# Kernel optimization log

Measured on AMD Instinct MI355X. Metric: run time of the kernel, lower is better.

The kernel has to match this reference:

```python
import jax, jax.numpy as jnp
import numpy as np

SR = 44100.0
MIN_GAIN, MAX_GAIN = -48.0, 12.0
MIN_EQ, MAX_EQ = -15.0, 15.0
MIN_CTS, MAX_CTS = -20.0, 10.0
# Freeverb (JUCE Reverb, as used by pedalboard.Reverb) tunings @ 44.1 kHz
COMB_T = [1116, 1188, 1277, 1356, 1422, 1491, 1557, 1617]
AP_T = [556, 441, 341, 225]
COMB_OFF = [0]
for _L in COMB_T:
    COMB_OFF.append(COMB_OFF[-1] + _L)
AP_OFF = [0]
for _L in AP_T:
    AP_OFF.append(AP_OFF[-1] + _L)


def restore(x, lo, hi):
    # inverse of normalize-to-(0,1)
    return x * (hi - lo) + lo


def first_order(fc, kind):
    # bilinear-transform 1st-order HP/LP (pedalboard High/LowpassFilter are 1st order)
    K = jnp.tan(np.pi * fc / SR)
    a1 = (K - 1.0) / (K + 1.0)
    z = jnp.zeros_like(fc)
    if kind == "hp":
        b0 = 1.0 / (1.0 + K)
        b = jnp.stack([b0, -b0, z], -1)
    else:
        b0 = K / (1.0 + K)
        b = jnp.stack([b0, b0, z], -1)
    a = jnp.stack([jnp.ones_like(fc), a1, z], -1)
    return b, a


def shelf(fc, gain_db, high):
    # RBJ cookbook shelf, Q = 1/sqrt(2)
    A = 10.0 ** (gain_db / 40.0)
    w = 2.0 * np.pi * fc / SR
    cw = jnp.cos(w)
    alpha = jnp.sin(w) * (np.sqrt(2.0) / 2.0)
    sq = 2.0 * jnp.sqrt(A) * alpha
    s = 1.0 if high else -1.0
    b0 = A * ((A + 1.0) + s * (A - 1.0) * cw + sq)
    b1 = -2.0 * s * A * ((A - 1.0) + s * (A + 1.0) * cw)
    b2 = A * ((A + 1.0) + s * (A - 1.0) * cw - sq)
    a0 = (A + 1.0) - s * (A - 1.0) * cw + sq
    a1 = 2.0 * s * ((A - 1.0) - s * (A + 1.0) * cw)
    a2 = (A + 1.0) - s * (A - 1.0) * cw - sq
    return jnp.stack([b0, b1, b2], -1), jnp.stack([a0, a1, a2], -1)


def peak(fc, gain_db, q):
    # RBJ cookbook peaking EQ
    A = 10.0 ** (gain_db / 40.0)
    w = 2.0 * np.pi * fc / SR
    cw = jnp.cos(w)
    alpha = jnp.sin(w) / (2.0 * q)
    b = jnp.stack([1.0 + alpha * A, -2.0 * cw, 1.0 - alpha * A], -1)
    a = jnp.stack([1.0 + alpha / A, -2.0 * cw, 1.0 - alpha / A], -1)
    return b, a


def cascade_biquads(x, B, A):
    # x: [N, T]; B, A: [N, 6, 3]. DF2T cascade of 6 sections via one scan.
    B = B / A[..., :1]
    A = A / A[..., :1]
    n_sec = B.shape[1]

    def step(z, xt):  # z: [N, 6, 2], xt: [N]
        s = xt
        zn = []
        for k in range(n_sec):
            y = B[:, k, 0] * s + z[:, k, 0]
            z1 = B[:, k, 1] * s - A[:, k, 1] * y + z[:, k, 1]
            z2 = B[:, k, 2] * s - A[:, k, 2] * y
            zn.append(jnp.stack([z1, z2], -1))
            s = y
        return jnp.stack(zn, 1), s

    z0 = jnp.zeros((x.shape[0], n_sec, 2), x.dtype)
    _, y = jax.lax.scan(step, z0, x.T)
    return y.T


def compressor(x, thr_db, ratio, att_ms, rel_ms):
    # feed-forward compressor, dB-domain gain computer + one-pole attack/release
    a_att = jnp.exp(-1.0 / (att_ms * 1e-3 * SR))  # [N]
    a_rel = jnp.exp(-1.0 / (rel_ms * 1e-3 * SR))
    lvl = 20.0 * jnp.log10(jnp.abs(x) + 1e-6)  # [N, T]
    tgt = jnp.minimum(0.0, (thr_db[:, None] - lvl) * (1.0 - 1.0 / ratio[:, None]))

    def step(g, t):  # g, t: [N] gain reduction in dB (<= 0)
        coef = jnp.where(t < g, a_att, a_rel)
        g = coef * g + (1.0 - coef) * t
        return g, g

    _, g = jax.lax.scan(step, jnp.zeros(x.shape[0], x.dtype), tgt.T)
    return x * 10.0 ** (g.T / 20.0)


def freeverb(x, room, damp01, wet, dry, width):
    # JUCE/Freeverb mono: 8 parallel damped combs -> 4 series allpasses
    fb = room * 0.28 + 0.7
    damp = damp01 * 0.4
    wet1 = 3.0 * wet * 0.5 * (1.0 + width)
    dryg = 2.0 * dry
    N = x.shape[0]
    CL, AL = COMB_OFF[-1], AP_OFF[-1]

    def step(carry, xt):
        cb, ab, st, t = carry
        inp = xt * 0.015
        acc = jnp.zeros_like(xt)
        st_new = []
        for k in range(8):
            idx = COMB_OFF[k] + t % COMB_T[k]
            out = cb[:, idx]
            s = out * (1.0 - damp) + st[:, k] * damp
            cb = cb.at[:, idx].set(inp + s * fb)
            st_new.append(s)
            acc = acc + out
        for k in range(4):
            idx = AP_OFF[k] + t % AP_T[k]
            buf = ab[:, idx]
            ab = ab.at[:, idx].set(acc + buf * 0.5)
            acc = buf - acc
        y = acc * wet1 + xt * dryg
        return (cb, ab, jnp.stack(st_new, 1), t + 1), y

    carry0 = (jnp.zeros((N, CL), x.dtype), jnp.zeros((N, AL), x.dtype),
              jnp.zeros((N, 8), x.dtype), jnp.int32(0))
    _, y = jax.lax.scan(step, carry0, x.T)
    return y.T


def _forward(x, p):
    bs, nt, T = x.shape
    N = bs * nt
    xf = x.reshape(N, T)
    pf = p.reshape(N, 24)

    gain_in = restore(pf[:, 0], MIN_GAIN, MAX_GAIN)
    xf = xf * (10.0 ** (gain_in / 20.0))[:, None]

    hp_fc = restore(pf[:, 1], 0.0, 350.0)
    lp_fc = restore(pf[:, 2], 3000.0, 22000.0)
    hs_fc = restore(pf[:, 3], 1500.0, 16000.0)
    hs_g = restore(pf[:, 4], MIN_EQ, MAX_EQ)
    ls_fc = restore(pf[:, 5], 30.0, 450.0)
    ls_g = restore(pf[:, 6], MIN_EQ, MAX_EQ)
    mh_fc = restore(pf[:, 7], 600.0, 7000.0)
    mh_g = restore(pf[:, 8], MIN_EQ, MAX_EQ)
    mh_q = restore(pf[:, 9], 0.5, 3.0)
    ml_fc = restore(pf[:, 10], 200.0, 2500.0)
    ml_g = restore(pf[:, 11], MIN_EQ, MAX_EQ)
    ml_q = restore(pf[:, 12], 0.5, 3.0)
    c_thr = restore(pf[:, 13], MIN_CTS, MAX_CTS)
    c_rat = restore(pf[:, 14], 1.0, 20.0)
    c_att = restore(pf[:, 15], 1.0, 30.0)
    c_rel = restore(pf[:, 16], 100.0, 4000.0)

    coefs = [first_order(hp_fc, "hp"), first_order(lp_fc, "lp"),
             shelf(hs_fc, hs_g, True), shelf(ls_fc, ls_g, False),
             peak(mh_fc, mh_g, mh_q), peak(ml_fc, ml_g, ml_q)]
    B = jnp.stack([c[0] for c in coefs], 1)  # [N, 6, 3]
    A = jnp.stack([c[1] for c in coefs], 1)
    xf = cascade_biquads(xf, B, A)
    xf = compressor(xf, c_thr, c_rat, c_att, c_rel)
    xf = freeverb(xf, pf[:, 17], pf[:, 18], pf[:, 19], pf[:, 20], pf[:, 21])

    gain_out = restore(pf[:, 22], MIN_GAIN, MAX_GAIN)
    xf = xf * (10.0 ** (gain_out / 20.0))[:, None]

    pan = restore(pf[:, 23], 0.3, 0.7)
    theta = pan * (np.pi / 2.0)
    pang = jnp.stack([jnp.cos(theta), jnp.sin(theta)], -1).reshape(bs, nt, 2)
    y = jnp.einsum("bnt,bnc->bct", xf.reshape(bs, nt, T), pang)

    p_out = jnp.stack([gain_in, hp_fc, lp_fc, hs_fc, hs_g, ls_fc, ls_g,
                       mh_fc, mh_g, mh_q, ml_fc, ml_g, ml_q,
                       c_thr, c_rat, c_att, c_rel,
                       pf[:, 17], pf[:, 18], pf[:, 19], pf[:, 20], pf[:, 21],
                       gain_out, pan], -1).reshape(bs, nt, 24)
    return y, p_out


_forward_jit = jax.jit(_forward)


def setup_inputs() -> dict:
    key = jax.random.key(0)
    k1, k2 = jax.random.split(key)
    x = 0.1 * jax.random.normal(k1, (4, 8, 65536), dtype=jnp.float32)
    p = jax.random.uniform(k2, (4, 8, 24), dtype=jnp.float32)
    return {"x": x, "p": p}


def reference(x, p):
    return _forward_jit(x, p)
```

## Files before the change

kernel.cpp:

```cpp
#include <hip/hip_runtime.h>
#include <math.h>

#define T 65536
#define NCH 32
#define LCHUNK 512
#define CCHUNK 128
#define SB 256
#define NBLK 256
#define VH 8

#define OFS_A  0
#define OFS_B1 2097152
#define OFS_I  4194304
#define OFS_P  7340032
#define OFS_M  7342080
#define OFS_V  7346688
#define OFS_Z  7395840


__device__ void norm_store(double b0,double b1,double b2,double a0,double a1,double a2,
                           double* B, double* A1, double* A2, int k){
  B[k*3+0]=b0/a0; B[k*3+1]=b1/a0; B[k*3+2]=b2/a0; A1[k]=a1/a0; A2[k]=a2/a0;
}

__device__ void shelf_coefs(double fc, double g, double s, double* B, double* A1, double* A2, int k){
  double A  = pow(10.0, g/40.0);
  double w  = 2.0*3.14159265358979323846*fc/44100.0;
  double cw = cos(w);
  double al = sin(w)*0.70710678118654752;
  double sq = 2.0*sqrt(A)*al;
  double b0 = A*((A+1.0) + s*(A-1.0)*cw + sq);
  double b1 = -2.0*s*A*((A-1.0) + s*(A+1.0)*cw);
  double b2 = A*((A+1.0) + s*(A-1.0)*cw - sq);
  double a0 = (A+1.0) - s*(A-1.0)*cw + sq;
  double a1 = 2.0*s*((A-1.0) - s*(A+1.0)*cw);
  double a2 = (A+1.0) - s*(A-1.0)*cw - sq;
  norm_store(b0,b1,b2,a0,a1,a2,B,A1,A2,k);
}

__device__ void peak_coefs(double fc, double g, double q, double* B, double* A1, double* A2, int k){
  double A  = pow(10.0, g/40.0);
  double w  = 2.0*3.14159265358979323846*fc/44100.0;
  double cw = cos(w);
  double al = sin(w)/(2.0*q);
  norm_store(1.0+al*A, -2.0*cw, 1.0-al*A, 1.0+al/A, -2.0*cw, 1.0-al/A, B,A1,A2,k);
}

__global__ void k_params(const float* __restrict__ p, float* __restrict__ ws, float* __restrict__ pout){
  int ch = threadIdx.x;
  if (ch >= NCH) return;
  const float* pf = p + ch*24;
  float f[24];
  #pragma unroll
  for (int j=0;j<24;j++) f[j]=pf[j];

  double gain_in = (double)f[0]*60.0 - 48.0;
  double hp_fc  = (double)f[1]*350.0;
  double lp_fc  = (double)f[2]*19000.0 + 3000.0;
  double hs_fc  = (double)f[3]*14500.0 + 1500.0;
  double hs_g   = (double)f[4]*30.0 - 15.0;
  double ls_fc  = (double)f[5]*420.0 + 30.0;
  double ls_g   = (double)f[6]*30.0 - 15.0;
  double mh_fc  = (double)f[7]*6400.0 + 600.0;
  double mh_g   = (double)f[8]*30.0 - 15.0;
  double mh_q   = (double)f[9]*2.5 + 0.5;
  double ml_fc  = (double)f[10]*2300.0 + 200.0;
  double ml_g   = (double)f[11]*30.0 - 15.0;
  double ml_q   = (double)f[12]*2.5 + 0.5;
  double c_thr  = (double)f[13]*30.0 - 20.0;
  double c_rat  = (double)f[14]*19.0 + 1.0;
  double c_att  = (double)f[15]*29.0 + 1.0;
  double c_rel  = (double)f[16]*3900.0 + 100.0;
  double gain_out=(double)f[22]*60.0 - 48.0;
  double pan    = (double)f[23]*0.4 + 0.3;

  double B[18], A1[6], A2[6];
  { double K = tan(3.14159265358979323846*hp_fc/44100.0);
    double a1=(K-1.0)/(K+1.0), b0=1.0/(1.0+K);
    B[0]=b0; B[1]=-b0; B[2]=0.0; A1[0]=a1; A2[0]=0.0; }
  { double K = tan(3.14159265358979323846*lp_fc/44100.0);
    double a1=(K-1.0)/(K+1.0), b0=K/(1.0+K);
    B[3]=b0; B[4]=b0; B[5]=0.0; A1[1]=a1; A2[1]=0.0; }
  shelf_coefs(hs_fc, hs_g,  1.0, B, A1, A2, 2);
  shelf_coefs(ls_fc, ls_g, -1.0, B, A1, A2, 3);
  peak_coefs (mh_fc, mh_g, mh_q, B, A1, A2, 4);
  peak_coefs (ml_fc, ml_g, ml_q, B, A1, A2, 5);

  double gin = pow(10.0, gain_in/20.0);
  B[0]*=gin; B[1]*=gin; B[2]*=gin;

  float* Pc = ws + OFS_P + ch*64;
  #pragma unroll
  for (int k=0;k<6;k++){
    Pc[k]    = (float)B[k*3+0];
    Pc[6+k]  = (float)B[k*3+1];
    Pc[12+k] = (float)B[k*3+2];
    Pc[18+k] = (float)A1[k];
    Pc[24+k] = (float)A2[k];
  }
  Pc[30] = (float)c_thr;
  Pc[31] = (float)(1.0 - 1.0/c_rat);
  Pc[32] = (float)exp(-1.0/(c_att*0.001*44100.0));
  Pc[33] = (float)exp(-1.0/(c_rel*0.001*44100.0));
  double fb   = (double)f[17]*0.28 + 0.7;
  double damp = (double)f[18]*0.4;
  double wet1 = 3.0*(double)f[19]*0.5*(1.0+(double)f[21]);
  double dryg = 2.0*(double)f[20];
  double gout = pow(10.0, gain_out/20.0);
  Pc[34] = (float)fb;
  Pc[35] = (float)damp;
  Pc[36] = (float)(wet1*gout);
  Pc[37] = (float)(dryg*gout/0.015);
  Pc[38] = (float)cos(pan*1.57079632679489662);
  Pc[39] = (float)sin(pan*1.57079632679489662);

  float* po = pout + ch*24;
  po[0]=(float)gain_in; po[1]=(float)hp_fc; po[2]=(float)lp_fc; po[3]=(float)hs_fc;
  po[4]=(float)hs_g; po[5]=(float)ls_fc; po[6]=(float)ls_g; po[7]=(float)mh_fc;
  po[8]=(float)mh_g; po[9]=(float)mh_q; po[10]=(float)ml_fc; po[11]=(float)ml_g;
  po[12]=(float)ml_q; po[13]=(float)c_thr; po[14]=(float)c_rat; po[15]=(float)c_att;
  po[16]=(float)c_rel; po[17]=f[17]; po[18]=f[18]; po[19]=f[19]; po[20]=f[20];
  po[21]=f[21]; po[22]=(float)gain_out; po[23]=(float)pan;
}


__device__ __forceinline__ float bq_step(const float* b0, const float* b1, const float* b2,
                                         const float* a1, const float* a2,
                                         float* z1, float* z2, float s){
  #pragma unroll
  for (int k=0;k<6;k++){
    float y = fmaf(b0[k], s, z1[k]);
    z1[k] = fmaf(b1[k], s, fmaf(-a1[k], y, z2[k]));
    z2[k] = fmaf(b2[k], s, -a2[k]*y);
    s = y;
  }
  return s;
}

__device__ __forceinline__ void load_coefs(const float* Pc, float* b0, float* b1, float* b2,
                                           float* a1, float* a2){
  #pragma unroll
  for (int k=0;k<6;k++){
    b0[k]=Pc[k]; b1[k]=Pc[6+k]; b2[k]=Pc[12+k]; a1[k]=Pc[18+k]; a2[k]=Pc[24+k];
  }
}

__global__ void k_chunk1(const float* __restrict__ x, float* __restrict__ ws){
  int tg = blockIdx.x*64 + threadIdx.x;
  int ch = tg / 140, sub = tg % 140;
  if (ch >= NCH) return;
  const float* Pc = ws + OFS_P + ch*64;
  float b0[6],b1[6],b2[6],a1[6],a2[6];
  load_coefs(Pc,b0,b1,b2,a1,a2);
  float z1[6]={0,0,0,0,0,0}, z2[6]={0,0,0,0,0,0};

  if (sub < CCHUNK){
    const float4* xp = (const float4*)(x + ch*T + sub*LCHUNK);
    for (int j=0;j<LCHUNK/4;j++){
      float4 v = xp[j];
      bq_step(b0,b1,b2,a1,a2,z1,z2,v.x);
      bq_step(b0,b1,b2,a1,a2,z1,z2,v.y);
      bq_step(b0,b1,b2,a1,a2,z1,z2,v.z);
      bq_step(b0,b1,b2,a1,a2,z1,z2,v.w);
    }
    float* vo = ws + OFS_V + (ch*CCHUNK + sub)*12;
    #pragma unroll
    for (int k=0;k<6;k++){ vo[2*k]=z1[k]; vo[2*k+1]=z2[k]; }
  } else {
    int j = sub - CCHUNK;
    if ((j & 1)==0) z1[j>>1]=1.0f; else z2[j>>1]=1.0f;
    for (int t=0;t<LCHUNK;t++) bq_step(b0,b1,b2,a1,a2,z1,z2,0.0f);
    float* mo = ws + OFS_M + ch*144 + j*12;
    #pragma unroll
    for (int k=0;k<6;k++){ mo[2*k]=z1[k]; mo[2*k+1]=z2[k]; }
  }
}

__global__ void k_chunk2(float* __restrict__ ws){
  int ch = threadIdx.x;
  if (ch >= NCH) return;
  const float* M = ws + OFS_M + ch*144;
  const float* V = ws + OFS_V + ch*CCHUNK*12;
  float*       Z = ws + OFS_Z + ch*CCHUNK*12;
  float z[12];
  #pragma unroll
  for (int i=0;i<12;i++) z[i]=0.0f;
  for (int c=0;c<CCHUNK;c++){
    #pragma unroll
    for (int i=0;i<12;i++) Z[c*12+i]=z[i];
    float zn[12];
    #pragma unroll
    for (int i=0;i<12;i++) zn[i]=V[c*12+i];
    #pragma unroll
    for (int j=0;j<12;j++){
      float zj = z[j];
      #pragma unroll
      for (int i=0;i<12;i++) zn[i] = fmaf(M[j*12+i], zj, zn[i]);
    }
    #pragma unroll
    for (int i=0;i<12;i++) z[i]=zn[i];
  }
}

__global__ void k_chunk3(const float* __restrict__ x, float* __restrict__ ws){
  int tg = blockIdx.x*64 + threadIdx.x;
  int ch = tg >> 7, c = tg & (CCHUNK-1);
  const float* Pc = ws + OFS_P + ch*64;
  float b0[6],b1[6],b2[6],a1[6],a2[6];
  load_coefs(Pc,b0,b1,b2,a1,a2);
  float thr = Pc[30], rt = Pc[31];
  float aA = Pc[32], aR = Pc[33];
  float kA = 1.0f - aA, kR = 1.0f - aR;
  const float* Zi = ws + OFS_Z + (ch*CCHUNK + c)*12;
  float z1[6], z2[6];
  #pragma unroll
  for (int k=0;k<6;k++){ z1[k]=Zi[2*k]; z2[k]=Zi[2*k+1]; }
  const float4* xp = (const float4*)(x + ch*T + c*LCHUNK);
  float4* Ao  = (float4*)(ws + OFS_A  + (size_t)ch*T + c*LCHUNK);
  float4* B1o = (float4*)(ws + OFS_B1 + (size_t)ch*T + c*LCHUNK);
  float*  Ig  = ws + OFS_I + (size_t)ch*98304;

  for (int gg=0; gg<64; gg++){
    float4 v0 = xp[2*gg], v1 = xp[2*gg+1];
    float ya[8], Tv[8];
    ya[0]=bq_step(b0,b1,b2,a1,a2,z1,z2,v0.x);
    ya[1]=bq_step(b0,b1,b2,a1,a2,z1,z2,v0.y);
    ya[2]=bq_step(b0,b1,b2,a1,a2,z1,z2,v0.z);
    ya[3]=bq_step(b0,b1,b2,a1,a2,z1,z2,v0.w);
    ya[4]=bq_step(b0,b1,b2,a1,a2,z1,z2,v1.x);
    ya[5]=bq_step(b0,b1,b2,a1,a2,z1,z2,v1.y);
    ya[6]=bq_step(b0,b1,b2,a1,a2,z1,z2,v1.z);
    ya[7]=bq_step(b0,b1,b2,a1,a2,z1,z2,v1.w);
    #pragma unroll
    for (int s=0;s<8;s++)
      Tv[s] = fminf(0.0f, (thr - 6.0205999132796239f*log2f(fabsf(ya[s])+1e-6f))*rt);
    Ao[2*gg]   = make_float4(ya[0],ya[1],ya[2],ya[3]);
    Ao[2*gg+1] = make_float4(ya[4],ya[5],ya[6],ya[7]);
    B1o[2*gg]   = make_float4(Tv[0],Tv[1],Tv[2],Tv[3]);
    B1o[2*gg+1] = make_float4(Tv[4],Tv[5],Tv[6],Tv[7]);
    float bb[9];
    bb[0] = kR*Tv[0]; bb[1] = kA*Tv[0];
    #pragma unroll
    for (int s=1;s<8;s++){
      float bA = kA*Tv[s], bR = kR*Tv[s];
      bb[s+1] = fmaf(aA, bb[s], bA);
      #pragma unroll
      for (int j=7;j>=1;j--){
        if (j<=s) bb[j] = fminf(fmaf(aA, bb[j-1], bA), fmaf(aR, bb[j], bR));
      }
      bb[0] = fmaf(aR, bb[0], bR);
    }
    int G = c*64 + gg;
    float* ig = Ig + (G>>5)*384 + (G&31)*12;
    *(float4*)(ig)   = make_float4(bb[0],bb[1],bb[2],bb[3]);
    *(float4*)(ig+4) = make_float4(bb[4],bb[5],bb[6],bb[7]);
    *(float4*)(ig+8) = make_float4(bb[8],0.0f,0.0f,0.0f);
  }
}


__global__ __launch_bounds__(320) void k_verb(float* __restrict__ ws){
  const int LC[8] = {1116,1188,1277,1356,1422,1491,1557,1617};
  const int COFF[8] = {0,1116,2304,3581,4937,6359,7850,9407};
  const int LA[4] = {556,441,341,225};
  const int AOFF[4] = {0,556,997,1338};
  int ch = blockIdx.x, tid = threadIdx.x;
  __shared__ float cb[11024];
  __shared__ float ab[1563];
  __shared__ float cH[8][264];
  __shared__ float xts[256];
  __shared__ float B1st[2][256];
  __shared__ float IldS[384];
  __shared__ float gB[2][32];
  __shared__ float xfer[32];
  const float* Pc = ws + OFS_P + ch*64;
  float fb = Pc[34], damp = Pc[35], wet1 = Pc[36], dryk = Pc[37];
  float aA = Pc[32], aR = Pc[33];
  float kA = 1.0f - aA, kR = 1.0f - aR;
  float omd = 1.0f - damp;
  float* Aio = ws + OFS_A + (size_t)ch*T;
  const float* B1c = ws + OFS_B1 + (size_t)ch*T;
  const float* IG  = ws + OFS_I + (size_t)ch*98304;
  for (int i=tid;i<11024;i+=320) cb[i]=0.0f;
  for (int i=tid;i<1563;i+=320)  ab[i]=0.0f;
  for (int i=tid;i<8*264;i+=320) ((float*)cH)[i]=0.0f;
  bool scanw = (tid >= 256);
  int sl = tid - 256;
  float w[VH];
  { float pw = 1.0f;
    #pragma unroll
    for (int d=0;d<VH;d++){ w[d]=pw; pw*=damp; } }
  float sj[9];
  { float pA = 1.0f;
    #pragma unroll
    for (int j=0;j<9;j++){ sj[j]=pA; pA*=aA; }
    float pR = 1.0f;
    #pragma unroll
    for (int j=8;j>=0;j--){ sj[j]*=pR; pR*=aR; } }
  int cbb[8] = {0,0,0,0,0,0,0,0};
  int abb[4] = {0,0,0,0};
  float gcarry = 0.0f;
  float4 iR0, iR1, bR;
  float xv = 0.0f;

  if (scanw){
    const float4* isrc = (const float4*)(IG);
    float4* idst = (float4*)IldS;
    idst[sl] = isrc[sl];
    if (sl < 32) idst[64+sl] = isrc[64+sl];
    iR0 = isrc[96+sl];
    if (sl < 32) iR1 = isrc[96+64+sl];
    const float4* bsrc = (const float4*)(B1c);
    ((float4*)B1st[0])[sl] = bsrc[sl];
    ((float4*)B1st[1])[sl] = bsrc[64+sl];
  }
  if (tid < 256) xv = Aio[tid];
  __syncthreads();
  if (tid == 256){
    float g = 0.0f;
    for (int m=0;m<32;m++){
      gB[0][m] = g;
      const float* Ip = &IldS[m*12];
      float f0=fmaf(sj[0],g,Ip[0]), f1=fmaf(sj[1],g,Ip[1]), f2=fmaf(sj[2],g,Ip[2]);
      float f3=fmaf(sj[3],g,Ip[3]), f4=fmaf(sj[4],g,Ip[4]), f5=fmaf(sj[5],g,Ip[5]);
      float f6=fmaf(sj[6],g,Ip[6]), f7=fmaf(sj[7],g,Ip[7]), f8=fmaf(sj[8],g,Ip[8]);
      g = fminf(fminf(fminf(f0,f1),fminf(f2,f3)),
                fminf(fminf(f4,f5),fminf(fminf(f6,f7),f8)));
    }
    gcarry = g;
  }
  __syncthreads();

  for (int i=0;i<NBLK;i++){
    int t0 = i<<8;
    int p = i & 1;
    float xt = 0.0f, acc = 0.0f, a = 0.0f;
    if (tid < 256){
      int m = tid>>3, r = tid&7;
      float g = gB[p][m];
      const float* Bl = B1st[p] + (m<<3);
      float4 q0 = *(const float4*)(Bl);
      float4 q1 = *(const float4*)(Bl+4);
      float tv[8] = {q0.x,q0.y,q0.z,q0.w,q1.x,q1.y,q1.z,q1.w};
      #pragma unroll
      for (int s=0;s<8;s++){
        if (s<=r){
          float tt = tv[s];
          g = fminf(fmaf(aA,g,kA*tt), fmaf(aR,g,kR*tt));
        }
      }
      xt = xv * exp2f(g*0.16609640474436813f) * 0.015f;
      xts[tid] = xt;
      #pragma unroll
      for (int k=0;k<8;k++){
        int idx = cbb[k]+tid; if (idx>=LC[k]) idx-=LC[k];
        float o = cb[COFF[k]+idx];
        cH[k][VH+tid] = omd*o;
        acc += o;
      }
    } else if (i+1 < NBLK){
      float4* idst = (float4*)IldS;
      idst[sl] = iR0;
      if (sl < 32) idst[64+sl] = iR1;
      if (i >= 1) ((float4*)B1st[(i+1)&1])[sl] = bR;
    }
    __syncthreads();
    if (tid < 256){
      if (i+1 < NBLK) xv = Aio[t0+256+tid];
      #pragma unroll
      for (int k=0;k<8;k++){
        float s = 0.0f;
        #pragma unroll
        for (int d=0;d<VH;d++) s = fmaf(w[d], cH[k][VH+tid-d], s);
        int idx = cbb[k]+tid; if (idx>=LC[k]) idx-=LC[k];
        cb[COFF[k]+idx] = fmaf(fb, s, xt);
      }
      a = acc;
      #pragma unroll
      for (int j=0;j<3;j++){
        int idx = abb[j]+tid; if (idx>=LA[j]) idx-=LA[j];
        float bv = ab[AOFF[j]+idx];
        ab[AOFF[j]+idx] = fmaf(0.5f, bv, a);
        a = bv - a;
      }
      if (tid >= 225) xfer[tid-225] = a;
    } else {
      if (i+2 < NBLK){
        const float4* isrc = (const float4*)(IG + (size_t)(i+2)*384);
        iR0 = isrc[sl];
        if (sl < 32) iR1 = isrc[64+sl];
        const float4* bsrc = (const float4*)(B1c + (size_t)(i+2)*SB);
        bR = bsrc[sl];
      }
      if (tid == 256 && i+1 < NBLK){
        int q = (i+1)&1;
        float g = gcarry;
        #pragma unroll 4
        for (int m=0;m<32;m++){
          gB[q][m] = g;
          const float* Ip = &IldS[m*12];
          float f0=fmaf(sj[0],g,Ip[0]), f1=fmaf(sj[1],g,Ip[1]), f2=fmaf(sj[2],g,Ip[2]);
          float f3=fmaf(sj[3],g,Ip[3]), f4=fmaf(sj[4],g,Ip[4]), f5=fmaf(sj[5],g,Ip[5]);
          float f6=fmaf(sj[6],g,Ip[6]), f7=fmaf(sj[7],g,Ip[7]), f8=fmaf(sj[8],g,Ip[8]);
          g = fminf(fminf(fminf(f0,f1),fminf(f2,f3)),
                    fminf(fminf(f4,f5),fminf(fminf(f6,f7),f8)));
        }
        gcarry = g;
      }
    }
    __syncthreads();
    if (tid < 225){
      int idx = abb[3]+tid; if (idx>=225) idx-=225;
      float bv = ab[AOFF[3]+idx];
      float b  = fmaf(0.5f, bv, a);
      float y  = bv - a;
      Aio[t0+tid] = fmaf(y, wet1, xts[tid]*dryk);
      if (tid < 31){
        float a2 = xfer[tid];
        float y2 = b - a2;
        ab[AOFF[3]+idx] = fmaf(0.5f, b, a2);
        Aio[t0+225+tid] = fmaf(y2, wet1, xts[225+tid]*dryk);
      } else {
        ab[AOFF[3]+idx] = b;
      }
    } else if (tid >= 232 && tid < 288){
      int q = tid-232; int k = q/7, d = q%7;
      cH[k][1+d] = cH[k][257+d];
    }
    #pragma unroll
    for (int k=0;k<8;k++){ cbb[k]+=SB; if (cbb[k]>=LC[k]) cbb[k]-=LC[k]; }
    #pragma unroll
    for (int j=0;j<4;j++){
      abb[j]+=SB;
      if (abb[j]>=LA[j]) abb[j]-=LA[j];
      if (abb[j]>=LA[j]) abb[j]-=LA[j];
    }
    __syncthreads();
  }
}


__global__ void k_mix(const float* __restrict__ ws, float* __restrict__ out){
  int id = blockIdx.x*256 + threadIdx.x;
  int t = id & (T-1), b = id >> 16;
  const float* Av = ws + OFS_A + (size_t)b*8*T + t;
  const float* P = ws + OFS_P;
  float s0=0.0f, s1=0.0f;
  #pragma unroll
  for (int n=0;n<8;n++){
    float v = Av[(size_t)n*T];
    int ch = b*8+n;
    s0 = fmaf(v, P[ch*64+38], s0);
    s1 = fmaf(v, P[ch*64+39], s1);
  }
  out[b*2*T + t]     = s0;
  out[b*2*T + T + t] = s1;
}

extern "C" void kernel_launch(void* const* d_in, const int* in_sizes, int n_in,
                              void* d_out, int out_size, void* d_ws, size_t ws_size,
                              hipStream_t stream) {
  const float* x = (const float*)d_in[0];
  const float* p = (const float*)d_in[1];
  float* out = (float*)d_out;
  float* ws  = (float*)d_ws;

  k_params<<<1, 64, 0, stream>>>(p, ws, out + 4*2*T);
  k_chunk1<<<70, 64, 0, stream>>>(x, ws);
  k_chunk2<<<1, 64, 0, stream>>>(ws);
  k_chunk3<<<64, 64, 0, stream>>>(x, ws);
  k_verb  <<<NCH, 320, 0, stream>>>(ws);
  k_mix   <<<(4*T)/256, 256, 0, stream>>>(ws, out);
}
```

Baseline: 962.5 us.

## Fuse parameter, chunked biquad scan, and reverb kernels into one per-channel kernel

```diff
diff --git a/kernel.cpp b/kernel.cpp
--- a/kernel.cpp
+++ b/kernel.cpp
@@ -13,17 +13,30 @@
 #define OFS_B1 2097152
 #define OFS_I  4194304
 #define OFS_P  7340032
-#define OFS_M  7342080
-#define OFS_V  7346688
-#define OFS_Z  7395840
-
-
-__device__ void norm_store(double b0,double b1,double b2,double a0,double a1,double a2,
-                           double* B, double* A1, double* A2, int k){
-  B[k*3+0]=b0/a0; B[k*3+1]=b1/a0; B[k*3+2]=b2/a0; A1[k]=a1/a0; A2[k]=a2/a0;
-}
-
-__device__ void shelf_coefs(double fc, double g, double s, double* B, double* A1, double* A2, int k){
+
+
+__device__ __forceinline__ float bq_step(const float* b0, const float* b1, const float* b2,
+                                         const float* a1, const float* a2,
+                                         float* z1, float* z2, float s){
+  #pragma unroll
+  for (int k=0;k<6;k++){
+    float y = fmaf(b0[k], s, z1[k]);
+    z1[k] = fmaf(b1[k], s, fmaf(-a1[k], y, z2[k]));
+    z2[k] = fmaf(b2[k], s, -a2[k]*y);
+    s = y;
+  }
+  return s;
+}
+
+__device__ __forceinline__ void load_coefs(const float* Pc, float* b0, float* b1, float* b2,
+                                           float* a1, float* a2){
+  #pragma unroll
+  for (int k=0;k<6;k++){
+    b0[k]=Pc[k]; b1[k]=Pc[6+k]; b2[k]=Pc[12+k]; a1[k]=Pc[18+k]; a2[k]=Pc[24+k];
+  }
+}
+
+__device__ void shelf_store(double fc, double g, double s, float* PcS, int k){
   double A  = pow(10.0, g/40.0);
   double w  = 2.0*3.14159265358979323846*fc/44100.0;
   double cw = cos(w);
@@ -35,231 +48,32 @@
   double a0 = (A+1.0) - s*(A-1.0)*cw + sq;
   double a1 = 2.0*s*((A-1.0) - s*(A+1.0)*cw);
   double a2 = (A+1.0) - s*(A-1.0)*cw - sq;
-  norm_store(b0,b1,b2,a0,a1,a2,B,A1,A2,k);
-}
-
-__device__ void peak_coefs(double fc, double g, double q, double* B, double* A1, double* A2, int k){
+  PcS[k]    = (float)(b0/a0);
+  PcS[6+k]  = (float)(b1/a0);
+  PcS[12+k] = (float)(b2/a0);
+  PcS[18+k] = (float)(a1/a0);
+  PcS[24+k] = (float)(a2/a0);
+}
+
+__device__ void peak_store(double fc, double g, double q, float* PcS, int k){
   double A  = pow(10.0, g/40.0);
   double w  = 2.0*3.14159265358979323846*fc/44100.0;
   double cw = cos(w);
   double al = sin(w)/(2.0*q);
-  norm_store(1.0+al*A, -2.0*cw, 1.0-al*A, 1.0+al/A, -2.0*cw, 1.0-al/A, B,A1,A2,k);
-}
-
-__global__ void k_params(const float* __restrict__ p, float* __restrict__ ws, float* __restrict__ pout){
-  int ch = threadIdx.x;
-  if (ch >= NCH) return;
-  const float* pf = p + ch*24;
-  float f[24];
-  #pragma unroll
-  for (int j=0;j<24;j++) f[j]=pf[j];
-
-  double gain_in = (double)f[0]*60.0 - 48.0;
-  double hp_fc  = (double)f[1]*350.0;
-  double lp_fc  = (double)f[2]*19000.0 + 3000.0;
-  double hs_fc  = (double)f[3]*14500.0 + 1500.0;
-  double hs_g   = (double)f[4]*30.0 - 15.0;
-  double ls_fc  = (double)f[5]*420.0 + 30.0;
-  double ls_g   = (double)f[6]*30.0 - 15.0;
-  double mh_fc  = (double)f[7]*6400.0 + 600.0;
-  double mh_g   = (double)f[8]*30.0 - 15.0;
-  double mh_q   = (double)f[9]*2.5 + 0.5;
-  double ml_fc  = (double)f[10]*2300.0 + 200.0;
-  double ml_g   = (double)f[11]*30.0 - 15.0;
-  double ml_q   = (double)f[12]*2.5 + 0.5;
-  double c_thr  = (double)f[13]*30.0 - 20.0;
-  double c_rat  = (double)f[14]*19.0 + 1.0;
-  double c_att  = (double)f[15]*29.0 + 1.0;
-  double c_rel  = (double)f[16]*3900.0 + 100.0;
-  double gain_out=(double)f[22]*60.0 - 48.0;
-  double pan    = (double)f[23]*0.4 + 0.3;
-
-  double B[18], A1[6], A2[6];
-  { double K = tan(3.14159265358979323846*hp_fc/44100.0);
-    double a1=(K-1.0)/(K+1.0), b0=1.0/(1.0+K);
-    B[0]=b0; B[1]=-b0; B[2]=0.0; A1[0]=a1; A2[0]=0.0; }
-  { double K = tan(3.14159265358979323846*lp_fc/44100.0);
-    double a1=(K-1.0)/(K+1.0), b0=K/(1.0+K);
-    B[3]=b0; B[4]=b0; B[5]=0.0; A1[1]=a1; A2[1]=0.0; }
-  shelf_coefs(hs_fc, hs_g,  1.0, B, A1, A2, 2);
-  shelf_coefs(ls_fc, ls_g, -1.0, B, A1, A2, 3);
-  peak_coefs (mh_fc, mh_g, mh_q, B, A1, A2, 4);
-  peak_coefs (ml_fc, ml_g, ml_q, B, A1, A2, 5);
-
-  double gin = pow(10.0, gain_in/20.0);
-  B[0]*=gin; B[1]*=gin; B[2]*=gin;
-
-  float* Pc = ws + OFS_P + ch*64;
-  #pragma unroll
-  for (int k=0;k<6;k++){
-    Pc[k]    = (float)B[k*3+0];
-    Pc[6+k]  = (float)B[k*3+1];
-    Pc[12+k] = (float)B[k*3+2];
-    Pc[18+k] = (float)A1[k];
-    Pc[24+k] = (float)A2[k];
-  }
-  Pc[30] = (float)c_thr;
-  Pc[31] = (float)(1.0 - 1.0/c_rat);
-  Pc[32] = (float)exp(-1.0/(c_att*0.001*44100.0));
-  Pc[33] = (float)exp(-1.0/(c_rel*0.001*44100.0));
-  double fb   = (double)f[17]*0.28 + 0.7;
-  double damp = (double)f[18]*0.4;
-  double wet1 = 3.0*(double)f[19]*0.5*(1.0+(double)f[21]);
-  double dryg = 2.0*(double)f[20];
-  double gout = pow(10.0, gain_out/20.0);
-  Pc[34] = (float)fb;
-  Pc[35] = (float)damp;
-  Pc[36] = (float)(wet1*gout);
-  Pc[37] = (float)(dryg*gout/0.015);
-  Pc[38] = (float)cos(pan*1.57079632679489662);
-  Pc[39] = (float)sin(pan*1.57079632679489662);
-
-  float* po = pout + ch*24;
-  po[0]=(float)gain_in; po[1]=(float)hp_fc; po[2]=(float)lp_fc; po[3]=(float)hs_fc;
-  po[4]=(float)hs_g; po[5]=(float)ls_fc; po[6]=(float)ls_g; po[7]=(float)mh_fc;
-  po[8]=(float)mh_g; po[9]=(float)mh_q; po[10]=(float)ml_fc; po[11]=(float)ml_g;
-  po[12]=(float)ml_q; po[13]=(float)c_thr; po[14]=(float)c_rat; po[15]=(float)c_att;
-  po[16]=(float)c_rel; po[17]=f[17]; po[18]=f[18]; po[19]=f[19]; po[20]=f[20];
-  po[21]=f[21]; po[22]=(float)gain_out; po[23]=(float)pan;
-}
-
-
-__device__ __forceinline__ float bq_step(const float* b0, const float* b1, const float* b2,
-                                         const float* a1, const float* a2,
-                                         float* z1, float* z2, float s){
-  #pragma unroll
-  for (int k=0;k<6;k++){
-    float y = fmaf(b0[k], s, z1[k]);
-    z1[k] = fmaf(b1[k], s, fmaf(-a1[k], y, z2[k]));
-    z2[k] = fmaf(b2[k], s, -a2[k]*y);
-    s = y;
-  }
-  return s;
-}
-
-__device__ __forceinline__ void load_coefs(const float* Pc, float* b0, float* b1, float* b2,
-                                           float* a1, float* a2){
-  #pragma unroll
-  for (int k=0;k<6;k++){
-    b0[k]=Pc[k]; b1[k]=Pc[6+k]; b2[k]=Pc[12+k]; a1[k]=Pc[18+k]; a2[k]=Pc[24+k];
-  }
-}
-
-__global__ void k_chunk1(const float* __restrict__ x, float* __restrict__ ws){
-  int tg = blockIdx.x*64 + threadIdx.x;
-  int ch = tg / 140, sub = tg % 140;
-  if (ch >= NCH) return;
-  const float* Pc = ws + OFS_P + ch*64;
-  float b0[6],b1[6],b2[6],a1[6],a2[6];
-  load_coefs(Pc,b0,b1,b2,a1,a2);
-  float z1[6]={0,0,0,0,0,0}, z2[6]={0,0,0,0,0,0};
-
-  if (sub < CCHUNK){
-    const float4* xp = (const float4*)(x + ch*T + sub*LCHUNK);
-    for (int j=0;j<LCHUNK/4;j++){
-      float4 v = xp[j];
-      bq_step(b0,b1,b2,a1,a2,z1,z2,v.x);
-      bq_step(b0,b1,b2,a1,a2,z1,z2,v.y);
-      bq_step(b0,b1,b2,a1,a2,z1,z2,v.z);
-      bq_step(b0,b1,b2,a1,a2,z1,z2,v.w);
-    }
-    float* vo = ws + OFS_V + (ch*CCHUNK + sub)*12;
-    #pragma unroll
-    for (int k=0;k<6;k++){ vo[2*k]=z1[k]; vo[2*k+1]=z2[k]; }
-  } else {
-    int j = sub - CCHUNK;
-    if ((j & 1)==0) z1[j>>1]=1.0f; else z2[j>>1]=1.0f;
-    for (int t=0;t<LCHUNK;t++) bq_step(b0,b1,b2,a1,a2,z1,z2,0.0f);
-    float* mo = ws + OFS_M + ch*144 + j*12;
-    #pragma unroll
-    for (int k=0;k<6;k++){ mo[2*k]=z1[k]; mo[2*k+1]=z2[k]; }
-  }
-}
-
-__global__ void k_chunk2(float* __restrict__ ws){
-  int ch = threadIdx.x;
-  if (ch >= NCH) return;
-  const float* M = ws + OFS_M + ch*144;
-  const float* V = ws + OFS_V + ch*CCHUNK*12;
-  float*       Z = ws + OFS_Z + ch*CCHUNK*12;
-  float z[12];
-  #pragma unroll
-  for (int i=0;i<12;i++) z[i]=0.0f;
-  for (int c=0;c<CCHUNK;c++){
-    #pragma unroll
-    for (int i=0;i<12;i++) Z[c*12+i]=z[i];
-    float zn[12];
-    #pragma unroll
-    for (int i=0;i<12;i++) zn[i]=V[c*12+i];
-    #pragma unroll
-    for (int j=0;j<12;j++){
-      float zj = z[j];
-      #pragma unroll
-      for (int i=0;i<12;i++) zn[i] = fmaf(M[j*12+i], zj, zn[i]);
-    }
-    #pragma unroll
-    for (int i=0;i<12;i++) z[i]=zn[i];
-  }
-}
-
-__global__ void k_chunk3(const float* __restrict__ x, float* __restrict__ ws){
-  int tg = blockIdx.x*64 + threadIdx.x;
-  int ch = tg >> 7, c = tg & (CCHUNK-1);
-  const float* Pc = ws + OFS_P + ch*64;
-  float b0[6],b1[6],b2[6],a1[6],a2[6];
-  load_coefs(Pc,b0,b1,b2,a1,a2);
-  float thr = Pc[30], rt = Pc[31];
-  float aA = Pc[32], aR = Pc[33];
-  float kA = 1.0f - aA, kR = 1.0f - aR;
-  const float* Zi = ws + OFS_Z + (ch*CCHUNK + c)*12;
-  float z1[6], z2[6];
-  #pragma unroll
-  for (int k=0;k<6;k++){ z1[k]=Zi[2*k]; z2[k]=Zi[2*k+1]; }
-  const float4* xp = (const float4*)(x + ch*T + c*LCHUNK);
-  float4* Ao  = (float4*)(ws + OFS_A  + (size_t)ch*T + c*LCHUNK);
-  float4* B1o = (float4*)(ws + OFS_B1 + (size_t)ch*T + c*LCHUNK);
-  float*  Ig  = ws + OFS_I + (size_t)ch*98304;
-
-  for (int gg=0; gg<64; gg++){
-    float4 v0 = xp[2*gg], v1 = xp[2*gg+1];
-    float ya[8], Tv[8];
-    ya[0]=bq_step(b0,b1,b2,a1,a2,z1,z2,v0.x);
-    ya[1]=bq_step(b0,b1,b2,a1,a2,z1,z2,v0.y);
-    ya[2]=bq_step(b0,b1,b2,a1,a2,z1,z2,v0.z);
-    ya[3]=bq_step(b0,b1,b2,a1,a2,z1,z2,v0.w);
-    ya[4]=bq_step(b0,b1,b2,a1,a2,z1,z2,v1.x);
-    ya[5]=bq_step(b0,b1,b2,a1,a2,z1,z2,v1.y);
-    ya[6]=bq_step(b0,b1,b2,a1,a2,z1,z2,v1.z);
-    ya[7]=bq_step(b0,b1,b2,a1,a2,z1,z2,v1.w);
-    #pragma unroll
-    for (int s=0;s<8;s++)
-      Tv[s] = fminf(0.0f, (thr - 6.0205999132796239f*log2f(fabsf(ya[s])+1e-6f))*rt);
-    Ao[2*gg]   = make_float4(ya[0],ya[1],ya[2],ya[3]);
-    Ao[2*gg+1] = make_float4(ya[4],ya[5],ya[6],ya[7]);
-    B1o[2*gg]   = make_float4(Tv[0],Tv[1],Tv[2],Tv[3]);
-    B1o[2*gg+1] = make_float4(Tv[4],Tv[5],Tv[6],Tv[7]);
-    float bb[9];
-    bb[0] = kR*Tv[0]; bb[1] = kA*Tv[0];
-    #pragma unroll
-    for (int s=1;s<8;s++){
-      float bA = kA*Tv[s], bR = kR*Tv[s];
-      bb[s+1] = fmaf(aA, bb[s], bA);
-      #pragma unroll
-      for (int j=7;j>=1;j--){
-        if (j<=s) bb[j] = fminf(fmaf(aA, bb[j-1], bA), fmaf(aR, bb[j], bR));
-      }
-      bb[0] = fmaf(aR, bb[0], bR);
-    }
-    int G = c*64 + gg;
-    float* ig = Ig + (G>>5)*384 + (G&31)*12;
-    *(float4*)(ig)   = make_float4(bb[0],bb[1],bb[2],bb[3]);
-    *(float4*)(ig+4) = make_float4(bb[4],bb[5],bb[6],bb[7]);
-    *(float4*)(ig+8) = make_float4(bb[8],0.0f,0.0f,0.0f);
-  }
-}
-
-
-__global__ __launch_bounds__(320) void k_verb(float* __restrict__ ws){
+  double b0 = 1.0+al*A, b1 = -2.0*cw, b2 = 1.0-al*A;
+  double a0 = 1.0+al/A, a1 = -2.0*cw, a2 = 1.0-al/A;
+  PcS[k]    = (float)(b0/a0);
+  PcS[6+k]  = (float)(b1/a0);
+  PcS[12+k] = (float)(b2/a0);
+  PcS[18+k] = (float)(a1/a0);
+  PcS[24+k] = (float)(a2/a0);
+}
+
+
+__global__ __launch_bounds__(320) void k_main(const float* __restrict__ x,
+                                              const float* __restrict__ p,
+                                              float* __restrict__ ws,
+                                              float* __restrict__ pout){
   const int LC[8] = {1116,1188,1277,1356,1422,1491,1557,1617};
   const int COFF[8] = {0,1116,2304,3581,4937,6359,7850,9407};
   const int LA[4] = {556,441,341,225};
@@ -273,14 +87,181 @@
   __shared__ float IldS[384];
   __shared__ float gB[2][32];
   __shared__ float xfer[32];
-  const float* Pc = ws + OFS_P + ch*64;
-  float fb = Pc[34], damp = Pc[35], wet1 = Pc[36], dryk = Pc[37];
-  float aA = Pc[32], aR = Pc[33];
-  float kA = 1.0f - aA, kR = 1.0f - aR;
-  float omd = 1.0f - damp;
+  float* Vls = cb;
+  float* Zls = cb + 1536;
+  float* Mls = cb + 3072;
+  float* PcS = cb + 3216;
+
   float* Aio = ws + OFS_A + (size_t)ch*T;
   const float* B1c = ws + OFS_B1 + (size_t)ch*T;
   const float* IG  = ws + OFS_I + (size_t)ch*98304;
+  const float* pf = p + ch*24;
+
+  if (tid == 0){
+    double gain_in = (double)pf[0]*60.0 - 48.0;
+    double hp_fc   = (double)pf[1]*350.0;
+    double gin = pow(10.0, gain_in/20.0);
+    double K = tan(3.14159265358979323846*hp_fc/44100.0);
+    double a1=(K-1.0)/(K+1.0), b0=1.0/(1.0+K);
+    PcS[0]  = (float)(b0*gin);
+    PcS[6]  = (float)(-b0*gin);
+    PcS[12] = 0.0f;
+    PcS[18] = (float)a1;
+    PcS[24] = 0.0f;
+  } else if (tid == 1){
+    double lp_fc = (double)pf[2]*19000.0 + 3000.0;
+    double K = tan(3.14159265358979323846*lp_fc/44100.0);
+    double a1=(K-1.0)/(K+1.0), b0=K/(1.0+K);
+    PcS[1]  = (float)b0;
+    PcS[7]  = (float)b0;
+    PcS[13] = 0.0f;
+    PcS[19] = (float)a1;
+    PcS[25] = 0.0f;
+  } else if (tid == 2){
+    shelf_store((double)pf[3]*14500.0 + 1500.0, (double)pf[4]*30.0 - 15.0,  1.0, PcS, 2);
+  } else if (tid == 3){
+    shelf_store((double)pf[5]*420.0 + 30.0,    (double)pf[6]*30.0 - 15.0, -1.0, PcS, 3);
+  } else if (tid == 4){
+    peak_store((double)pf[7]*6400.0 + 600.0,  (double)pf[8]*30.0 - 15.0,
+               (double)pf[9]*2.5 + 0.5, PcS, 4);
+  } else if (tid == 5){
+    peak_store((double)pf[10]*2300.0 + 200.0, (double)pf[11]*30.0 - 15.0,
+               (double)pf[12]*2.5 + 0.5, PcS, 5);
+  } else if (tid == 6){
+    double c_thr = (double)pf[13]*30.0 - 20.0;
+    double c_rat = (double)pf[14]*19.0 + 1.0;
+    double c_att = (double)pf[15]*29.0 + 1.0;
+    double c_rel = (double)pf[16]*3900.0 + 100.0;
+    PcS[30] = (float)c_thr;
+    PcS[31] = (float)(1.0 - 1.0/c_rat);
+    PcS[32] = (float)exp(-1.0/(c_att*0.001*44100.0));
+    PcS[33] = (float)exp(-1.0/(c_rel*0.001*44100.0));
+  } else if (tid == 7){
+    double fb   = (double)pf[17]*0.28 + 0.7;
+    double damp = (double)pf[18]*0.4;
+    double wet1 = 3.0*(double)pf[19]*0.5*(1.0+(double)pf[21]);
+    double dryg = 2.0*(double)pf[20];
+    double gain_out = (double)pf[22]*60.0 - 48.0;
+    double gout = pow(10.0, gain_out/20.0);
+    double pan  = (double)pf[23]*0.4 + 0.3;
+    PcS[34] = (float)fb;
+    PcS[35] = (float)damp;
+    PcS[36] = (float)(wet1*gout);
+    PcS[37] = (float)(dryg*gout/0.015);
+    PcS[38] = (float)cos(pan*1.57079632679489662);
+    PcS[39] = (float)sin(pan*1.57079632679489662);
+  } else if (tid == 8){
+    float* po = pout + ch*24;
+    po[0]=(float)((double)pf[0]*60.0-48.0);   po[1]=(float)((double)pf[1]*350.0);
+    po[2]=(float)((double)pf[2]*19000.0+3000.0); po[3]=(float)((double)pf[3]*14500.0+1500.0);
+    po[4]=(float)((double)pf[4]*30.0-15.0);   po[5]=(float)((double)pf[5]*420.0+30.0);
+    po[6]=(float)((double)pf[6]*30.0-15.0);   po[7]=(float)((double)pf[7]*6400.0+600.0);
+    po[8]=(float)((double)pf[8]*30.0-15.0);   po[9]=(float)((double)pf[9]*2.5+0.5);
+    po[10]=(float)((double)pf[10]*2300.0+200.0); po[11]=(float)((double)pf[11]*30.0-15.0);
+    po[12]=(float)((double)pf[12]*2.5+0.5);   po[13]=(float)((double)pf[13]*30.0-20.0);
+    po[14]=(float)((double)pf[14]*19.0+1.0);  po[15]=(float)((double)pf[15]*29.0+1.0);
+    po[16]=(float)((double)pf[16]*3900.0+100.0);
+    po[17]=pf[17]; po[18]=pf[18]; po[19]=pf[19]; po[20]=pf[20]; po[21]=pf[21];
+    po[22]=(float)((double)pf[22]*60.0-48.0); po[23]=(float)((double)pf[23]*0.4+0.3);
+  }
+  __syncthreads();
+
+  float fb = PcS[34], damp = PcS[35], wet1 = PcS[36], dryk = PcS[37];
+  float aA = PcS[32], aR = PcS[33];
+  float thr = PcS[30], rt = PcS[31];
+  float kA = 1.0f - aA, kR = 1.0f - aR;
+  float omd = 1.0f - damp;
+  float b0[6],b1[6],b2[6],a1[6],a2[6];
+  if (tid < 140) load_coefs(PcS,b0,b1,b2,a1,a2);
+  if (tid < 40) (ws + OFS_P + ch*64)[tid] = PcS[tid];
+
+  if (tid < 140){
+    float z1[6]={0,0,0,0,0,0}, z2[6]={0,0,0,0,0,0};
+    if (tid < CCHUNK){
+      const float4* xp = (const float4*)(x + ch*T + tid*LCHUNK);
+      for (int j=0;j<LCHUNK/4;j++){
+        float4 v = xp[j];
+        bq_step(b0,b1,b2,a1,a2,z1,z2,v.x);
+        bq_step(b0,b1,b2,a1,a2,z1,z2,v.y);
+        bq_step(b0,b1,b2,a1,a2,z1,z2,v.z);
+        bq_step(b0,b1,b2,a1,a2,z1,z2,v.w);
+      }
+      #pragma unroll
+      for (int k=0;k<6;k++){ Vls[tid*12+2*k]=z1[k]; Vls[tid*12+2*k+1]=z2[k]; }
+    } else {
+      int j = tid - CCHUNK;
+      if ((j & 1)==0) z1[j>>1]=1.0f; else z2[j>>1]=1.0f;
+      for (int t=0;t<LCHUNK;t++) bq_step(b0,b1,b2,a1,a2,z1,z2,0.0f);
+      #pragma unroll
+      for (int k=0;k<6;k++){ Mls[j*12+2*k]=z1[k]; Mls[j*12+2*k+1]=z2[k]; }
+    }
+  }
+  __syncthreads();
+
+  if (tid < 64){
+    int i = tid; bool act = (i < 12);
+    float Mr_[12];
+    #pragma unroll
+    for (int j=0;j<12;j++) Mr_[j] = act ? Mls[j*12+i] : 0.0f;
+    float z = 0.0f;
+    for (int c=0;c<CCHUNK;c++){
+      if (act) Zls[c*12+i] = z;
+      float zn = act ? Vls[c*12+i] : 0.0f;
+      #pragma unroll
+      for (int j=0;j<12;j++) zn = fmaf(Mr_[j], __shfl(z, j), zn);
+      z = zn;
+    }
+  }
+  __syncthreads();
+
+  if (tid < CCHUNK){
+    int c = tid;
+    float z1[6], z2[6];
+    #pragma unroll
+    for (int k=0;k<6;k++){ z1[k]=Zls[c*12+2*k]; z2[k]=Zls[c*12+2*k+1]; }
+    const float4* xp = (const float4*)(x + ch*T + c*LCHUNK);
+    float4* Ao  = (float4*)(ws + OFS_A  + (size_t)ch*T + c*LCHUNK);
+    float4* B1o = (float4*)(ws + OFS_B1 + (size_t)ch*T + c*LCHUNK);
+    float*  Ig  = ws + OFS_I + (size_t)ch*98304;
+    for (int gg=0; gg<64; gg++){
+      float4 v0 = xp[2*gg], v1 = xp[2*gg+1];
+      float ya[8], Tv[8];
+      ya[0]=bq_step(b0,b1,b2,a1,a2,z1,z2,v0.x);
+      ya[1]=bq_step(b0,b1,b2,a1,a2,z1,z2,v0.y);
+      ya[2]=bq_step(b0,b1,b2,a1,a2,z1,z2,v0.z);
+      ya[3]=bq_step(b0,b1,b2,a1,a2,z1,z2,v0.w);
+      ya[4]=bq_step(b0,b1,b2,a1,a2,z1,z2,v1.x);
+      ya[5]=bq_step(b0,b1,b2,a1,a2,z1,z2,v1.y);
+      ya[6]=bq_step(b0,b1,b2,a1,a2,z1,z2,v1.z);
+      ya[7]=bq_step(b0,b1,b2,a1,a2,z1,z2,v1.w);
+      #pragma unroll
+      for (int s=0;s<8;s++)
+        Tv[s] = fminf(0.0f, (thr - 6.0205999132796239f*log2f(fabsf(ya[s])+1e-6f))*rt);
+      Ao[2*gg]   = make_float4(ya[0],ya[1],ya[2],ya[3]);
+      Ao[2*gg+1] = make_float4(ya[4],ya[5],ya[6],ya[7]);
+      B1o[2*gg]   = make_float4(Tv[0],Tv[1],Tv[2],Tv[3]);
+      B1o[2*gg+1] = make_float4(Tv[4],Tv[5],Tv[6],Tv[7]);
+      float bb[9];
+      bb[0] = kR*Tv[0]; bb[1] = kA*Tv[0];
+      #pragma unroll
+      for (int s=1;s<8;s++){
+        float bA = kA*Tv[s], bR = kR*Tv[s];
+        bb[s+1] = fmaf(aA, bb[s], bA);
+        #pragma unroll
+        for (int j=7;j>=1;j--){
+          if (j<=s) bb[j] = fminf(fmaf(aA, bb[j-1], bA), fmaf(aR, bb[j], bR));
+        }
+        bb[0] = fmaf(aR, bb[0], bR);
+      }
+      int G = c*64 + gg;
+      float* ig = Ig + (G>>5)*384 + (G&31)*12;
+      *(float4*)(ig)   = make_float4(bb[0],bb[1],bb[2],bb[3]);
+      *(float4*)(ig+4) = make_float4(bb[4],bb[5],bb[6],bb[7]);
+      *(float4*)(ig+8) = make_float4(bb[8],0.0f,0.0f,0.0f);
+    }
+  }
+  __syncthreads();
+
   for (int i=tid;i<11024;i+=320) cb[i]=0.0f;
   for (int i=tid;i<1563;i+=320)  ab[i]=0.0f;
   for (int i=tid;i<8*264;i+=320) ((float*)cH)[i]=0.0f;
@@ -333,12 +314,12 @@
 
   for (int i=0;i<NBLK;i++){
     int t0 = i<<8;
-    int p = i & 1;
+    int p2 = i & 1;
     float xt = 0.0f, acc = 0.0f, a = 0.0f;
     if (tid < 256){
       int m = tid>>3, r = tid&7;
-      float g = gB[p][m];
-      const float* Bl = B1st[p] + (m<<3);
+      float g = gB[p2][m];
+      const float* Bl = B1st[p2] + (m<<3);
       float4 q0 = *(const float4*)(Bl);
       float4 q1 = *(const float4*)(Bl+4);
       float tv[8] = {q0.x,q0.y,q0.z,q0.w,q1.x,q1.y,q1.z,q1.w};
@@ -416,9 +397,9 @@
       float y  = bv - a;
       Aio[t0+tid] = fmaf(y, wet1, xts[tid]*dryk);
       if (tid < 31){
-        float a2 = xfer[tid];
-        float y2 = b - a2;
-        ab[AOFF[3]+idx] = fmaf(0.5f, b, a2);
+        float a2v = xfer[tid];
+        float y2 = b - a2v;
+        ab[AOFF[3]+idx] = fmaf(0.5f, b, a2v);
         Aio[t0+225+tid] = fmaf(y2, wet1, xts[225+tid]*dryk);
       } else {
         ab[AOFF[3]+idx] = b;
@@ -465,10 +446,6 @@
   float* out = (float*)d_out;
   float* ws  = (float*)d_ws;
 
-  k_params<<<1, 64, 0, stream>>>(p, ws, out + 4*2*T);
-  k_chunk1<<<70, 64, 0, stream>>>(x, ws);
-  k_chunk2<<<1, 64, 0, stream>>>(ws);
-  k_chunk3<<<64, 64, 0, stream>>>(x, ws);
-  k_verb  <<<NCH, 320, 0, stream>>>(ws);
-  k_mix   <<<(4*T)/256, 256, 0, stream>>>(ws, out);
-}
+  k_main<<<NCH, 320, 0, stream>>>(x, p, ws, out + 4*2*T);
+  k_mix <<<(4*T)/256, 256, 0, stream>>>(ws, out);
+}
```

Measured after the change: 841.2 us. 12.6% less time.
